# Kernel tuning notes

Hardware: AMD Instinct MI355X
Metric: run time of the kernel (lower is better)

The kernel has to match this reference:

```python
import jax, jax.numpy as jnp
import numpy as np

B, D = 128, 512
ORDER, DEPTH = 1, 2


def setup_inputs() -> dict:
    key = jax.random.key(0)
    kx, kw = jax.random.split(key)
    x = jax.random.normal(kx, (B, D), dtype=jnp.float32)
    # scale the cubic meta-weight so repeated contractions stay O(1)
    W = jax.random.normal(kw, (D, D, D), dtype=jnp.float32) * (1.0 / np.sqrt(D))
    bias = jnp.zeros((D,), dtype=jnp.float32)
    return {"x": x, "W": W, "bias": bias}


def reference(x, W, bias):
    # Meta-linear: per-sample effective weight obtained by contracting the
    # trailing `ORDER` modes of W (out, in, in, ...) with x, rescaled by
    # 1/sqrt(d) per contraction, then applied as a linear layer; repeat DEPTH times.
    sqrt_d = np.sqrt(x.shape[-1]).astype(np.float32)
    for _ in range(DEPTH):
        # first contraction introduces the batch dim: (out, in, k) x (b, k) -> (b, out, in)
        w = jnp.einsum('...k,bk->b...', W, x) / sqrt_d
        for _ in range(ORDER - 1):
            w = jnp.einsum('b...k,bk->b...', w, x) / sqrt_d
        x = jnp.einsum('boi,bi->bo', w, x) + bias
    return x
```

## Files before the change

kernel.cpp:

```cpp
#include <hip/hip_runtime.h>
#include <hip/hip_fp16.h>


typedef __attribute__((ext_vector_type(8))) _Float16 f16x8;
typedef __attribute__((ext_vector_type(4))) float    f32x4v;
typedef __attribute__((ext_vector_type(2))) unsigned u32x2;
typedef __attribute__((ext_vector_type(4))) unsigned u32x4;

#define DD 512
#define BB 128
#define INV_SQRT_D 0.04419417382415922f

static __device__ __forceinline__ unsigned pkh(float a, float b) {
    __half2 h = __float22half2_rn(make_float2(a, b));
    unsigned u; __builtin_memcpy(&u, &h, sizeof(u)); return u;
}
static __device__ __forceinline__ u32x4 pack8(f32x4v a, f32x4v b) {
    u32x4 r; r.x = pkh(a.x, a.y); r.y = pkh(a.z, a.w);
             r.z = pkh(b.x, b.y); r.w = pkh(b.z, b.w); return r;
}
static __device__ __forceinline__ f16x8 as_h8(u32x4 q) {
    f16x8 v; __builtin_memcpy(&v, &q, sizeof(v)); return v;
}

__global__ __launch_bounds__(256, 4)
void metagemm(const float* __restrict__ x, const float* __restrict__ W,
              float* __restrict__ part) {
    __shared__ u32x4    kp_lds[1024];
    __shared__ unsigned sc_lds[4096];
    __shared__ u32x2    wt_lds[4][256];

    const int tid  = threadIdx.x;
    const int lane = tid & 63;
    const int wv   = tid >> 6;
    const int bid  = blockIdx.x;
    const int ob   = bid >> 7;
    const int ig   = (bid >> 3) & 15;
    const int kp   = bid & 7;

    const int o0   = ob * 64 + wv * 16;
    const int i0   = ig * 32;
    const int kb   = kp * 64;
    const int l15  = lane & 15;
    const int quad = lane >> 4;

    const int lr = lane >> 4;
    const int lc = lane & 15;
    const float* wp0 = W + (long)(o0 + 0 + lr) * (DD * DD) + (long)i0 * DD + kb + lc * 4;
    const float* wp1 = W + (long)(o0 + 4 + lr) * (DD * DD) + (long)i0 * DD + kb + lc * 4;
    const float* wp2 = W + (long)(o0 + 8 + lr) * (DD * DD) + (long)i0 * DD + kb + lc * 4;
    const float* wp3 = W + (long)(o0 + 12 + lr) * (DD * DD) + (long)i0 * DD + kb + lc * 4;

    u32x2* wtw0 = &wt_lds[wv][(0 + lr) * 16 + (((lc >> 1) ^ ((0 + lr) & 7)) * 2) + (lc & 1)];
    u32x2* wtw1 = &wt_lds[wv][(4 + lr) * 16 + (((lc >> 1) ^ ((4 + lr) & 7)) * 2) + (lc & 1)];
    u32x2* wtw2 = &wt_lds[wv][(8 + lr) * 16 + (((lc >> 1) ^ ((8 + lr) & 7)) * 2) + (lc & 1)];
    u32x2* wtw3 = &wt_lds[wv][(12 + lr) * 16 + (((lc >> 1) ^ ((12 + lr) & 7)) * 2) + (lc & 1)];
    const u32x4* wtr = (const u32x4*)&wt_lds[wv][0];
    const u32x4* wtr0 = wtr + l15 * 8 + ((0 * 4 + quad) ^ (l15 & 7));
    const u32x4* wtr1 = wtr + l15 * 8 + ((1 * 4 + quad) ^ (l15 & 7));

    f32x4v p0a = *(const f32x4v*)(wp0);
    f32x4v p0b = *(const f32x4v*)(wp1);
    f32x4v p0c = *(const f32x4v*)(wp2);
    f32x4v p0d = *(const f32x4v*)(wp3);
    f32x4v p1a = *(const f32x4v*)(wp0 + DD);
    f32x4v p1b = *(const f32x4v*)(wp1 + DD);
    f32x4v p1c = *(const f32x4v*)(wp2 + DD);
    f32x4v p1d = *(const f32x4v*)(wp3 + DD);

    const int koff = quad * 8;
#pragma unroll
    for (int ff = 0; ff < 2; ++ff) {
        const int f   = wv * 2 + ff;
        const int row = f * 16 + l15;
        const float* xr = x + row * DD + kb + koff;
#pragma unroll
        for (int ks = 0; ks < 2; ++ks) {
            f32x4v a = *(const f32x4v*)(xr + ks * 32);
            f32x4v b = *(const f32x4v*)(xr + ks * 32 + 4);
            kp_lds[(ks * 8 + f) * 64 + lane] = pack8(a, b);
        }
    }
    {
        const int row  = tid & 127;
        const int half = tid >> 7;
#pragma unroll
        for (int c4 = 0; c4 < 4; ++c4) {
            const int i = half * 16 + c4 * 4;
            f32x4v v = *(const f32x4v*)(x + row * DD + i0 + i);
#pragma unroll
            for (int j = 0; j < 4; ++j) {
                float s = v[j] * INV_SQRT_D;
                sc_lds[(i + j) * 128 + row] = pkh(s, s);
            }
        }
    }
    __syncthreads();

    f32x4v c[8];
#pragma unroll
    for (int f = 0; f < 8; ++f) c[f] = (f32x4v){0.f, 0.f, 0.f, 0.f};

    unsigned lic = 0;
#pragma unroll 1
    for (int n = 0; n < 32; ++n) {
        asm volatile("" : "+v"(lic));

        f32x4v ca = p0a, cb = p0b, cc = p0c, cd = p0d;
        p0a = p1a; p0b = p1b; p0c = p1c; p0d = p1d;
        if (n < 30) {
            const long off = (long)(n + 2) * DD;
            p1a = *(const f32x4v*)(wp0 + off);
            p1b = *(const f32x4v*)(wp1 + off);
            p1c = *(const f32x4v*)(wp2 + off);
            p1d = *(const f32x4v*)(wp3 + off);
        }

        *wtw0 = (u32x2){pkh(ca.x, ca.y), pkh(ca.z, ca.w)};
        *wtw1 = (u32x2){pkh(cb.x, cb.y), pkh(cb.z, cb.w)};
        *wtw2 = (u32x2){pkh(cc.x, cc.y), pkh(cc.z, cc.w)};
        *wtw3 = (u32x2){pkh(cd.x, cd.y), pkh(cd.z, cd.w)};

        const unsigned* scp = sc_lds + n * 128 + l15 + lic;
        const u32x4*    kpp = kp_lds + lane + lic;

        f16x8 bf0 = as_h8(wtr0[lic]);
        f16x8 bf1 = as_h8(wtr1[lic]);

#pragma unroll
        for (int f = 0; f < 8; ++f) {
            unsigned su = scp[f * 16];
            u32x4 sq = {su, su, su, su};
            f16x8 sv = as_h8(sq);
            f16x8 a0 = as_h8(kpp[f * 64]) * sv;
            c[f] = __builtin_amdgcn_mfma_f32_16x16x32_f16(a0, bf0, c[f], 0, 0, 0);
            f16x8 a1 = as_h8(kpp[(8 + f) * 64]) * sv;
            c[f] = __builtin_amdgcn_mfma_f32_16x16x32_f16(a1, bf1, c[f], 0, 0, 0);
        }
    }

    float* pbase = part + (long)(ig * 8 + kp) * (BB * DD) + ob * 64;
    const int ocol = wv * 16 + l15;
#pragma unroll
    for (int f = 0; f < 8; ++f) {
#pragma unroll
        for (int r = 0; r < 4; ++r) {
            pbase[(f * 16 + quad * 4 + r) * DD + ocol] = c[f][r];
        }
    }
}

__global__ void reduce_bias(const float* __restrict__ part, const float* __restrict__ bias,
                            float* __restrict__ out) {
    const int idx = blockIdx.x * 256 + threadIdx.x;
    float s = bias[idx & (DD - 1)];
#pragma unroll 16
    for (int p = 0; p < 128; ++p) s += part[(long)p * (BB * DD) + idx];
    out[idx] = s;
}

extern "C" void kernel_launch(void* const* d_in, const int* in_sizes, int n_in,
                              void* d_out, int out_size, void* d_ws, size_t ws_size,
                              hipStream_t stream) {
    (void)in_sizes; (void)n_in; (void)out_size; (void)ws_size;

    const float* x    = (const float*)d_in[0];
    const float* W    = (const float*)d_in[1];
    const float* bias = (const float*)d_in[2];
    float* out = (float*)d_out;

    float* part = (float*)d_ws;
    float* x1   = part + 128 * BB * DD;

    metagemm<<<1024, 256, 0, stream>>>(x, W, part);
    reduce_bias<<<(BB * DD) / 256, 256, 0, stream>>>(part, bias, x1);

    metagemm<<<1024, 256, 0, stream>>>(x1, W, part);
    reduce_bias<<<(BB * DD) / 256, 256, 0, stream>>>(part, bias, out);
}
```

Before: 826.9 us.

## Restructure meta-linear into W·x GEMM then per-output reduction with x

Replaces the fused per-block triple contraction with a two-stage scheme. A prep kernel makes a scaled fp16 copy of x and a transposed fp32 copy. Stage one treats W as a (D*D)×D matrix, multiplies it by x on MFMA, and writes an fp16 intermediate V of size D*D×B. Stage two contracts V with x over the inner index and adds the bias. The goal is to avoid the 128-way partial-sum buffer and its reduction pass, and to simplify operand reuse. The cost is a large fp16 intermediate written and read back through global memory (about 64 MB per layer), plus extra fp16 rounding of V.

```diff
diff --git a/kernel.cpp b/kernel.cpp
--- a/kernel.cpp
+++ b/kernel.cpp
@@ -22,141 +22,165 @@
 static __device__ __forceinline__ f16x8 as_h8(u32x4 q) {
     f16x8 v; __builtin_memcpy(&v, &q, sizeof(v)); return v;
 }
-
-__global__ __launch_bounds__(256, 4)
-void metagemm(const float* __restrict__ x, const float* __restrict__ W,
-              float* __restrict__ part) {
-    __shared__ u32x4    kp_lds[1024];
-    __shared__ unsigned sc_lds[4096];
-    __shared__ u32x2    wt_lds[4][256];
+static __device__ __forceinline__ float2 h2f(unsigned u) {
+    __half2 h; __builtin_memcpy(&h, &u, 4); return __half22float2(h);
+}
+
+__global__ void prep(const float* __restrict__ x, u32x4* __restrict__ xhf,
+                     float* __restrict__ xT) {
+    const int t = blockIdx.x * 256 + threadIdx.x;
+    if (t < 8192) {
+        const int lane = t & 63, fid = t >> 6;
+        const int kw = fid >> 3, nf = fid & 7;
+        const int b  = nf * 16 + (lane & 15);
+        const int k0 = kw * 32 + (lane >> 4) * 8;
+        const float* xr = x + b * DD + k0;
+        f32x4v a = *(const f32x4v*)(xr)     * INV_SQRT_D;
+        f32x4v c = *(const f32x4v*)(xr + 4) * INV_SQRT_D;
+        xhf[t] = pack8(a, c);
+    } else {
+        const int u = t - 8192;
+        const int i = u >> 5, c4 = u & 31;
+        f32x4v v;
+        v.x = x[(c4 * 4 + 0) * DD + i];
+        v.y = x[(c4 * 4 + 1) * DD + i];
+        v.z = x[(c4 * 4 + 2) * DD + i];
+        v.w = x[(c4 * 4 + 3) * DD + i];
+        *(f32x4v*)(xT + i * BB + c4 * 4) = v;
+    }
+}
+
+__global__ __launch_bounds__(256, 2)
+void s1_gemm(const float* __restrict__ W, const u32x4* __restrict__ xhf,
+             unsigned* __restrict__ V32) {
+    __shared__ u32x4    abuf[2048];
+    __shared__ unsigned vbuf[2][2048];
 
     const int tid  = threadIdx.x;
     const int lane = tid & 63;
     const int wv   = tid >> 6;
-    const int bid  = blockIdx.x;
-    const int ob   = bid >> 7;
-    const int ig   = (bid >> 3) & 15;
-    const int kp   = bid & 7;
-
-    const int o0   = ob * 64 + wv * 16;
-    const int i0   = ig * 32;
-    const int kb   = kp * 64;
     const int l15  = lane & 15;
     const int quad = lane >> 4;
-
-    const int lr = lane >> 4;
-    const int lc = lane & 15;
-    const float* wp0 = W + (long)(o0 + 0 + lr) * (DD * DD) + (long)i0 * DD + kb + lc * 4;
-    const float* wp1 = W + (long)(o0 + 4 + lr) * (DD * DD) + (long)i0 * DD + kb + lc * 4;
-    const float* wp2 = W + (long)(o0 + 8 + lr) * (DD * DD) + (long)i0 * DD + kb + lc * 4;
-    const float* wp3 = W + (long)(o0 + 12 + lr) * (DD * DD) + (long)i0 * DD + kb + lc * 4;
-
-    u32x2* wtw0 = &wt_lds[wv][(0 + lr) * 16 + (((lc >> 1) ^ ((0 + lr) & 7)) * 2) + (lc & 1)];
-    u32x2* wtw1 = &wt_lds[wv][(4 + lr) * 16 + (((lc >> 1) ^ ((4 + lr) & 7)) * 2) + (lc & 1)];
-    u32x2* wtw2 = &wt_lds[wv][(8 + lr) * 16 + (((lc >> 1) ^ ((8 + lr) & 7)) * 2) + (lc & 1)];
-    u32x2* wtw3 = &wt_lds[wv][(12 + lr) * 16 + (((lc >> 1) ^ ((12 + lr) & 7)) * 2) + (lc & 1)];
-    const u32x4* wtr = (const u32x4*)&wt_lds[wv][0];
-    const u32x4* wtr0 = wtr + l15 * 8 + ((0 * 4 + quad) ^ (l15 & 7));
-    const u32x4* wtr1 = wtr + l15 * 8 + ((1 * 4 + quad) ^ (l15 & 7));
-
-    f32x4v p0a = *(const f32x4v*)(wp0);
-    f32x4v p0b = *(const f32x4v*)(wp1);
-    f32x4v p0c = *(const f32x4v*)(wp2);
-    f32x4v p0d = *(const f32x4v*)(wp3);
-    f32x4v p1a = *(const f32x4v*)(wp0 + DD);
-    f32x4v p1b = *(const f32x4v*)(wp1 + DD);
-    f32x4v p1c = *(const f32x4v*)(wp2 + DD);
-    f32x4v p1d = *(const f32x4v*)(wp3 + DD);
-
-    const int koff = quad * 8;
-#pragma unroll
-    for (int ff = 0; ff < 2; ++ff) {
-        const int f   = wv * 2 + ff;
-        const int row = f * 16 + l15;
-        const float* xr = x + row * DD + kb + koff;
-#pragma unroll
-        for (int ks = 0; ks < 2; ++ks) {
-            f32x4v a = *(const f32x4v*)(xr + ks * 32);
-            f32x4v b = *(const f32x4v*)(xr + ks * 32 + 4);
-            kp_lds[(ks * 8 + f) * 64 + lane] = pack8(a, b);
-        }
-    }
-    {
-        const int row  = tid & 127;
-        const int half = tid >> 7;
-#pragma unroll
-        for (int c4 = 0; c4 < 4; ++c4) {
-            const int i = half * 16 + c4 * 4;
-            f32x4v v = *(const f32x4v*)(x + row * DD + i0 + i);
-#pragma unroll
-            for (int j = 0; j < 4; ++j) {
-                float s = v[j] * INV_SQRT_D;
-                sc_lds[(i + j) * 128 + row] = pkh(s, s);
-            }
-        }
-    }
-    __syncthreads();
-
-    f32x4v c[8];
-#pragma unroll
-    for (int f = 0; f < 8; ++f) c[f] = (f32x4v){0.f, 0.f, 0.f, 0.f};
+    const int sw   = l15 & 7;
+
+    const long rowbase = (long)blockIdx.x * 256;
+    const float* wp = W + rowbase * DD + (wv * 8) * DD + lane * 4;
+
+    f32x4v g[16];
+#pragma unroll
+    for (int j = 0; j < 16; ++j)
+        g[j] = *(const f32x4v*)(wp + (j >> 1) * DD + (j & 1) * 256);
+#pragma unroll
+    for (int j = 0; j < 16; ++j) {
+        const int row = wv * 8 + (j >> 1);
+        const int c8  = (j & 1) * 64 + lane;
+        const int c16 = c8 >> 1;
+        ((u32x2*)abuf)[(row * 64 + (c16 ^ (row & 7))) * 2 + (c8 & 1)] =
+            (u32x2){pkh(g[j].x, g[j].y), pkh(g[j].z, g[j].w)};
+    }
 
     unsigned lic = 0;
 #pragma unroll 1
+    for (int s = 0; s < 8; ++s) {
+        asm volatile("" : "+v"(lic));
+        __syncthreads();
+
+        if (s < 7) {
+            const float* wps = wp + (long)(s + 1) * 32 * DD;
+#pragma unroll
+            for (int j = 0; j < 16; ++j)
+                g[j] = *(const f32x4v*)(wps + (j >> 1) * DD + (j & 1) * 256);
+        }
+
+        f32x4v c00 = {0,0,0,0}, c01 = {0,0,0,0}, c10 = {0,0,0,0}, c11 = {0,0,0,0};
+        const u32x4* bp  = xhf + (wv * 2) * 64 + lane + lic;
+        const u32x4* a0p = abuf + l15 * 64;
+        const u32x4* a1p = abuf + (16 + l15) * 64;
+#pragma unroll 4
+        for (int kw = 0; kw < 16; ++kw) {
+            f16x8 b0 = as_h8(bp[(kw * 8 + 0) * 64]);
+            f16x8 b1 = as_h8(bp[(kw * 8 + 1) * 64]);
+            f16x8 a0 = as_h8(a0p[(kw * 4 + quad) ^ sw]);
+            f16x8 a1 = as_h8(a1p[(kw * 4 + quad) ^ sw]);
+            c00 = __builtin_amdgcn_mfma_f32_16x16x32_f16(a0, b0, c00, 0, 0, 0);
+            c01 = __builtin_amdgcn_mfma_f32_16x16x32_f16(a0, b1, c01, 0, 0, 0);
+            c10 = __builtin_amdgcn_mfma_f32_16x16x32_f16(a1, b0, c10, 0, 0, 0);
+            c11 = __builtin_amdgcn_mfma_f32_16x16x32_f16(a1, b1, c11, 0, 0, 0);
+        }
+
+        unsigned short* vb = (unsigned short*)vbuf[s & 1];
+        const int bcol = wv * 32 + l15;
+#pragma unroll
+        for (int r = 0; r < 4; ++r) {
+            const int rw0 = (quad * 4 + r) * BB;
+            const int rw1 = (16 + quad * 4 + r) * BB;
+            __half h;
+            h = __float2half_rn(c00[r]); __builtin_memcpy(&vb[rw0 + bcol],      &h, 2);
+            h = __float2half_rn(c01[r]); __builtin_memcpy(&vb[rw0 + bcol + 16], &h, 2);
+            h = __float2half_rn(c10[r]); __builtin_memcpy(&vb[rw1 + bcol],      &h, 2);
+            h = __float2half_rn(c11[r]); __builtin_memcpy(&vb[rw1 + bcol + 16], &h, 2);
+        }
+
+        __syncthreads();
+
+        if (s < 7) {
+#pragma unroll
+            for (int j = 0; j < 16; ++j) {
+                const int row = wv * 8 + (j >> 1);
+                const int c8  = (j & 1) * 64 + lane;
+                const int c16 = c8 >> 1;
+                ((u32x2*)abuf)[(row * 64 + (c16 ^ (row & 7))) * 2 + (c8 & 1)] =
+                    (u32x2){pkh(g[j].x, g[j].y), pkh(g[j].z, g[j].w)};
+            }
+        }
+
+        const unsigned* vbr = vbuf[s & 1];
+        unsigned* vout = V32 + (rowbase + s * 32 + wv * 8) * 64 + lane;
+#pragma unroll
+        for (int r = 0; r < 8; ++r)
+            vout[r * 64] = vbr[(wv * 8 + r) * 64 + lane];
+    }
+}
+
+__global__ __launch_bounds__(256, 2)
+void s2_reduce(const unsigned* __restrict__ V32, const float* __restrict__ xT,
+               const float* __restrict__ bias, float* __restrict__ out) {
+    __shared__ float2 red[4][64];
+    const int tid = threadIdx.x, lane = tid & 63, wv = tid >> 6;
+    const int o = blockIdx.x;
+    const unsigned* vp = V32 + (long)o * DD * 64 + wv * 64 + lane;
+    const float*    xp = xT + wv * BB + 2 * lane;
+
+    float2 a0 = {0,0}, a1 = {0,0}, a2 = {0,0}, a3 = {0,0};
+#pragma unroll 2
     for (int n = 0; n < 32; ++n) {
-        asm volatile("" : "+v"(lic));
-
-        f32x4v ca = p0a, cb = p0b, cc = p0c, cd = p0d;
-        p0a = p1a; p0b = p1b; p0c = p1c; p0d = p1d;
-        if (n < 30) {
-            const long off = (long)(n + 2) * DD;
-            p1a = *(const f32x4v*)(wp0 + off);
-            p1b = *(const f32x4v*)(wp1 + off);
-            p1c = *(const f32x4v*)(wp2 + off);
-            p1d = *(const f32x4v*)(wp3 + off);
-        }
-
-        *wtw0 = (u32x2){pkh(ca.x, ca.y), pkh(ca.z, ca.w)};
-        *wtw1 = (u32x2){pkh(cb.x, cb.y), pkh(cb.z, cb.w)};
-        *wtw2 = (u32x2){pkh(cc.x, cc.y), pkh(cc.z, cc.w)};
-        *wtw3 = (u32x2){pkh(cd.x, cd.y), pkh(cd.z, cd.w)};
-
-        const unsigned* scp = sc_lds + n * 128 + l15 + lic;
-        const u32x4*    kpp = kp_lds + lane + lic;
-
-        f16x8 bf0 = as_h8(wtr0[lic]);
-        f16x8 bf1 = as_h8(wtr1[lic]);
-
-#pragma unroll
-        for (int f = 0; f < 8; ++f) {
-            unsigned su = scp[f * 16];
-            u32x4 sq = {su, su, su, su};
-            f16x8 sv = as_h8(sq);
-            f16x8 a0 = as_h8(kpp[f * 64]) * sv;
-            c[f] = __builtin_amdgcn_mfma_f32_16x16x32_f16(a0, bf0, c[f], 0, 0, 0);
-            f16x8 a1 = as_h8(kpp[(8 + f) * 64]) * sv;
-            c[f] = __builtin_amdgcn_mfma_f32_16x16x32_f16(a1, bf1, c[f], 0, 0, 0);
-        }
-    }
-
-    float* pbase = part + (long)(ig * 8 + kp) * (BB * DD) + ob * 64;
-    const int ocol = wv * 16 + l15;
-#pragma unroll
-    for (int f = 0; f < 8; ++f) {
-#pragma unroll
-        for (int r = 0; r < 4; ++r) {
-            pbase[(f * 16 + quad * 4 + r) * DD + ocol] = c[f][r];
-        }
-    }
-}
-
-__global__ void reduce_bias(const float* __restrict__ part, const float* __restrict__ bias,
-                            float* __restrict__ out) {
-    const int idx = blockIdx.x * 256 + threadIdx.x;
-    float s = bias[idx & (DD - 1)];
-#pragma unroll 16
-    for (int p = 0; p < 128; ++p) s += part[(long)p * (BB * DD) + idx];
-    out[idx] = s;
+        unsigned v0 = vp[(4 * n + 0) * 256];
+        unsigned v1 = vp[(4 * n + 1) * 256];
+        unsigned v2 = vp[(4 * n + 2) * 256];
+        unsigned v3 = vp[(4 * n + 3) * 256];
+        float2 x0 = *(const float2*)(xp + (4 * n + 0) * 512);
+        float2 x1 = *(const float2*)(xp + (4 * n + 1) * 512);
+        float2 x2 = *(const float2*)(xp + (4 * n + 2) * 512);
+        float2 x3 = *(const float2*)(xp + (4 * n + 3) * 512);
+        float2 f;
+        f = h2f(v0); a0.x += f.x * x0.x; a0.y += f.y * x0.y;
+        f = h2f(v1); a1.x += f.x * x1.x; a1.y += f.y * x1.y;
+        f = h2f(v2); a2.x += f.x * x2.x; a2.y += f.y * x2.y;
+        f = h2f(v3); a3.x += f.x * x3.x; a3.y += f.y * x3.y;
+    }
+    float2 acc;
+    acc.x = (a0.x + a1.x) + (a2.x + a3.x);
+    acc.y = (a0.y + a1.y) + (a2.y + a3.y);
+    red[wv][lane] = acc;
+    __syncthreads();
+    if (wv == 0) {
+        float2 s0 = red[0][lane], s1 = red[1][lane], s2 = red[2][lane], s3 = red[3][lane];
+        float sx = (s0.x + s1.x) + (s2.x + s3.x);
+        float sy = (s0.y + s1.y) + (s2.y + s3.y);
+        float bo = bias[o];
+        out[(2 * lane)     * DD + o] = sx + bo;
+        out[(2 * lane + 1) * DD + o] = sy + bo;
+    }
 }
 
 extern "C" void kernel_launch(void* const* d_in, const int* in_sizes, int n_in,
@@ -169,12 +193,16 @@
     const float* bias = (const float*)d_in[2];
     float* out = (float*)d_out;
 
-    float* part = (float*)d_ws;
-    float* x1   = part + 128 * BB * DD;
-
-    metagemm<<<1024, 256, 0, stream>>>(x, W, part);
-    reduce_bias<<<(BB * DD) / 256, 256, 0, stream>>>(part, bias, x1);
-
-    metagemm<<<1024, 256, 0, stream>>>(x1, W, part);
-    reduce_bias<<<(BB * DD) / 256, 256, 0, stream>>>(part, bias, out);
-}
+    unsigned* V32 = (unsigned*)d_ws;
+    u32x4*    xhf = (u32x4*)((char*)d_ws + (size_t)262144 * 64 * 4);
+    float*    xT  = (float*)((char*)xhf + 8192 * sizeof(u32x4));
+    float*    x1  = xT + DD * BB;
+
+    prep<<<96, 256, 0, stream>>>(x, xhf, xT);
+    s1_gemm<<<1024, 256, 0, stream>>>(W, xhf, V32);
+    s2_reduce<<<512, 256, 0, stream>>>(V32, xT, bias, x1);
+
+    prep<<<96, 256, 0, stream>>>(x1, xhf, xT);
+    s1_gemm<<<1024, 256, 0, stream>>>(W, xhf, V32);
+    s2_reduce<<<512, 256, 0, stream>>>(V32, xT, bias, out);
+}
```

New measurement: 883.7 us. 6.9% more time.
